# Kernel tuning notes

Hardware: AMD Instinct MI355X
Metric: run time of the kernel (lower is better)

## Reference

```python
import jax, jax.numpy as jnp
import numpy as np

N_NODES = 50000
N_EDGES = 800000
IN_DIM = 128
HID = 32
HEADS = 8
N_CLASSES = 10
N_GRAPHS = 64
NEG_SLOPE = 0.2


def _lin(key, fan_in, fan_out):
    return jax.random.normal(key, (fan_in, fan_out), jnp.float32) / np.sqrt(fan_in)


def setup_inputs() -> dict:
    key = jax.random.key(0)
    ks = jax.random.split(key, 24)
    x = jax.random.normal(ks[0], (N_NODES, IN_DIM), jnp.float32)
    edge_index = jax.random.randint(ks[1], (2, N_EDGES), 0, N_NODES, jnp.int64)
    batch = jnp.sort(jax.random.randint(ks[2], (N_NODES,), 0, N_GRAPHS, jnp.int64))
    HC = HEADS * HID
    return {
        "x": x,
        "edge_index": edge_index,
        "batch": batch,
        # GATConv(IN_DIM, HID, heads=8): shared lin, att_src/att_dst, bias on concat output
        "gat_W": _lin(ks[3], IN_DIM, HC),
        "gat_att_src": jax.random.normal(ks[4], (HEADS, HID), jnp.float32) / np.sqrt(HID),
        "gat_att_dst": jax.random.normal(ks[5], (HEADS, HID), jnp.float32) / np.sqrt(HID),
        "gat_b": jnp.zeros((HC,), jnp.float32),
        # GraphConv(HC, HID): lin_rel (bias) on aggregated neighbors + lin_root (no bias)
        "W2_rel": _lin(ks[6], HC, HID), "b2": jnp.zeros((HID,), jnp.float32), "W2_root": _lin(ks[7], HC, HID),
        # SAGEConv(HID, HID): lin_l (bias) on mean-aggregated neighbors + lin_r (no bias)
        "W3_l": _lin(ks[8], HID, HID), "b3": jnp.zeros((HID,), jnp.float32), "W3_r": _lin(ks[9], HID, HID),
        # GraphConv(HID, HID)
        "W4_rel": _lin(ks[10], HID, HID), "b4": jnp.zeros((HID,), jnp.float32), "W4_root": _lin(ks[11], HID, HID),
        "fc1_W": _lin(ks[12], HID, HID), "fc1_b": jnp.zeros((HID,), jnp.float32),
        "fc2_W": _lin(ks[13], HID, N_CLASSES), "fc2_b": jnp.zeros((N_CLASSES,), jnp.float32),
    }


def _segment_softmax(logits, seg_ids, num_segments):
    # numerically-stable softmax over edges grouped by destination node
    m = jax.ops.segment_max(logits, seg_ids, num_segments=num_segments)
    e = jnp.exp(logits - m[seg_ids])
    z = jax.ops.segment_sum(e, seg_ids, num_segments=num_segments)
    return e / (z[seg_ids] + 1e-16)


def _gnn_forward(x, edge_index, batch, gat_W, gat_att_src, gat_att_dst, gat_b,
                 W2_rel, b2, W2_root, W3_l, b3, W3_r, W4_rel, b4, W4_root,
                 fc1_W, fc1_b, fc2_W, fc2_b):
    N = x.shape[0]
    src0, dst0 = edge_index[0], edge_index[1]

    # ---- GATConv (PyG defaults: add_self_loops=True, concat heads, neg_slope=0.2) ----
    loops = jnp.arange(N)
    src = jnp.concatenate([src0, loops])
    dst = jnp.concatenate([dst0, loops])
    h = (x @ gat_W).reshape(N, HEADS, HID)                 # [N,H,C]
    a_src = jnp.sum(h * gat_att_src, axis=-1)              # [N,H]
    a_dst = jnp.sum(h * gat_att_dst, axis=-1)              # [N,H]
    logits = jax.nn.leaky_relu(a_src[src] + a_dst[dst], NEG_SLOPE)  # [E',H]
    alpha = _segment_softmax(logits, dst, N)               # [E',H]
    msg = h[src] * alpha[:, :, None]                       # [E',H,C]
    out = jax.ops.segment_sum(msg, dst, num_segments=N).reshape(N, HEADS * HID) + gat_b
    x1 = jax.nn.relu(out)

    # ---- GraphConv (aggr='add'): lin_rel(sum_j x_j) + lin_root(x) ----
    agg = jax.ops.segment_sum(x1[src0], dst0, num_segments=N)
    x2 = jax.nn.relu(agg @ W2_rel + b2 + x1 @ W2_root)

    # ---- SAGEConv (aggr='mean'): lin_l(mean_j x_j) + lin_r(x) ----
    deg = jax.ops.segment_sum(jnp.ones((src0.shape[0],), x2.dtype), dst0, num_segments=N)
    agg = jax.ops.segment_sum(x2[src0], dst0, num_segments=N) / jnp.clip(deg, 1.0)[:, None]
    x3 = jax.nn.relu(agg @ W3_l + b3 + x2 @ W3_r)

    # ---- GraphConv ----
    agg = jax.ops.segment_sum(x3[src0], dst0, num_segments=N)
    x4 = jax.nn.relu(agg @ W4_rel + b4 + x3 @ W4_root)

    # ---- global_mean_pool + MLP head ----
    gsum = jax.ops.segment_sum(x4, batch, num_segments=N_GRAPHS)
    gcnt = jax.ops.segment_sum(jnp.ones((N,), x4.dtype), batch, num_segments=N_GRAPHS)
    g = gsum / jnp.clip(gcnt, 1.0)[:, None]                # [G,HID]
    g = jax.nn.relu(g @ fc1_W + fc1_b)
    return g @ fc2_W + fc2_b                               # [G, N_CLASSES]


def reference(x, edge_index, batch, gat_W, gat_att_src, gat_att_dst, gat_b,
              W2_rel, b2, W2_root, W3_l, b3, W3_r, W4_rel, b4, W4_root,
              fc1_W, fc1_b, fc2_W, fc2_b):
    return _gnn_forward(x, edge_index, batch, gat_W, gat_att_src, gat_att_dst, gat_b,
                        W2_rel, b2, W2_root, W3_l, b3, W3_r, W4_rel, b4, W4_root,
                        fc1_W, fc1_b, fc2_W, fc2_b)
```

## Files before the change

### kernel.cpp

```cpp
#include <hip/hip_runtime.h>

#define IN_DIM 128
#define HID 32
#define HEADS 8
#define HC 256
#define N_GRAPHS 64
#define N_CLASSES 10

#define SCAN_ELEMS 8
#define SCAN_BLOCK 256
#define SCAN_CHUNK (SCAN_ELEMS * SCAN_BLOCK)

typedef __attribute__((ext_vector_type(8))) short bf16x8;
typedef __attribute__((ext_vector_type(4))) float f32x4;

__device__ __forceinline__ float leaky(float v) { return v > 0.f ? v : 0.2f * v; }

__device__ __forceinline__ unsigned fenc(float f) {
    unsigned u = __float_as_uint(f);
    return (u & 0x80000000u) ? ~u : (u | 0x80000000u);
}
__device__ __forceinline__ float fdec(unsigned u) {
    return __uint_as_float((u & 0x80000000u) ? (u & 0x7FFFFFFFu) : ~u);
}
__device__ __forceinline__ unsigned short bf16r(float f) {
    unsigned u = __float_as_uint(f);
    return (unsigned short)((u + 0x7FFFu + ((u >> 16) & 1u)) >> 16);
}
__device__ __forceinline__ float bdec(unsigned short u) {
    return __uint_as_float(((unsigned)u) << 16);
}

__global__ __launch_bounds__(256) void k_setup(
    int* __restrict__ deg, int N, unsigned* __restrict__ gm,
    float* __restrict__ gsum, float* __restrict__ gcnt, int* __restrict__ counter,
    const float* __restrict__ W, const float* __restrict__ Wrel, const float* __restrict__ Wroot,
    unsigned short* __restrict__ Wb, unsigned short* __restrict__ W2b)
{
    int i = blockIdx.x * 256 + threadIdx.x;
    if (i < N) deg[i] = 0;
    if (i < HEADS) gm[i] = 0u;
    if (i < N_GRAPHS * HID) gsum[i] = 0.f;
    if (i < N_GRAPHS) gcnt[i] = 0.f;
    if (i == 0) *counter = 0;

    if (blockIdx.x < 16) {
        int slot = blockIdx.x * 256 + threadIdx.x;
        int lane = slot & 63;
        int ctg  = (slot >> 6) & 15;
        int ks   = slot >> 10;
        int col  = ctg * 16 + (lane & 15);
        int kb   = ks * 32 + (lane >> 4) * 8;
        unsigned short t[8];
#pragma unroll
        for (int j = 0; j < 8; ++j) t[j] = bf16r(W[(size_t)(kb + j) * HC + col]);
        ushort4* dst = (ushort4*)(Wb + (size_t)slot * 8);
        dst[0] = make_ushort4(t[0], t[1], t[2], t[3]);
        dst[1] = make_ushort4(t[4], t[5], t[6], t[7]);
    } else if (blockIdx.x < 24) {
        int slot = (blockIdx.x - 16) * 256 + threadIdx.x;
        int lane = slot & 63;
        int ct   = (slot >> 6) & 3;
        int ks   = slot >> 8;
        int col  = ct * 16 + (lane & 15);
        int kb   = ks * 32 + (lane >> 4) * 8;
        const float* src = (col < HID) ? (Wrel + col) : (Wroot + (col - HID));
        unsigned short t[8];
#pragma unroll
        for (int j = 0; j < 8; ++j) t[j] = bf16r(src[(size_t)(kb + j) * HID]);
        ushort4* dst = (ushort4*)(W2b + (size_t)slot * 8);
        dst[0] = make_ushort4(t[0], t[1], t[2], t[3]);
        dst[1] = make_ushort4(t[4], t[5], t[6], t[7]);
    }
}

__global__ __launch_bounds__(256) void k_gemm_deg(
    const float* __restrict__ x, const unsigned short* __restrict__ Wb,
    const float* __restrict__ att_s, const float* __restrict__ att_d,
    unsigned short* __restrict__ h, float* __restrict__ a_src, float* __restrict__ a_dst, int N,
    const int* __restrict__ edst, int* __restrict__ deg, unsigned short* __restrict__ rank,
    int E, int gemmBlocks)
{
    __shared__ unsigned short sxt[16][136];
    __shared__ unsigned short sh[4][16][72];
    if (blockIdx.x >= gemmBlocks) {
        int i = (blockIdx.x - gemmBlocks) * 256 + threadIdx.x;
        if (i < E) rank[i] = (unsigned short)atomicAdd(&deg[edst[i]], 1);
        return;
    }
    int w = threadIdx.x >> 6;
    int lane = threadIdx.x & 63;
    int lrow = lane & 15, lgrp = lane >> 4;
    int nb = blockIdx.x * 16;

    {
        int row = threadIdx.x >> 4, col = (threadIdx.x & 15) * 8;
        int n = min(nb + row, N - 1);
        const float* xp = x + (size_t)n * IN_DIM + col;
        float4 a0 = *(const float4*)xp;
        float4 a1 = *(const float4*)(xp + 4);
        *(ushort4*)(&sxt[row][col])     = make_ushort4(bf16r(a0.x), bf16r(a0.y), bf16r(a0.z), bf16r(a0.w));
        *(ushort4*)(&sxt[row][col + 4]) = make_ushort4(bf16r(a1.x), bf16r(a1.y), bf16r(a1.z), bf16r(a1.w));
    }
    __syncthreads();

    f32x4 acc0 = {0.f, 0.f, 0.f, 0.f}, acc1 = acc0, acc2 = acc0, acc3 = acc0;

#pragma unroll
    for (int ks = 0; ks < 4; ++ks) {
        bf16x8 af = *(const bf16x8*)(&sxt[lrow][ks * 32 + lgrp * 8]);
        const bf16x8* bp = (const bf16x8*)(Wb + ((size_t)(ks * 16 + w * 4) * 64 + lane) * 8);
        acc0 = __builtin_amdgcn_mfma_f32_16x16x32_bf16(af, bp[0 * 64], acc0, 0, 0, 0);
        acc1 = __builtin_amdgcn_mfma_f32_16x16x32_bf16(af, bp[1 * 64], acc1, 0, 0, 0);
        acc2 = __builtin_amdgcn_mfma_f32_16x16x32_bf16(af, bp[2 * 64], acc2, 0, 0, 0);
        acc3 = __builtin_amdgcn_mfma_f32_16x16x32_bf16(af, bp[3 * 64], acc3, 0, 0, 0);
    }

    int cbase = w * 64;
#pragma unroll
    for (int r = 0; r < 4; ++r) {
        int lr = lgrp * 4 + r;
        sh[w][lr][lrow]      = bf16r(acc0[r]);
        sh[w][lr][16 + lrow] = bf16r(acc1[r]);
        sh[w][lr][32 + lrow] = bf16r(acc2[r]);
        sh[w][lr][48 + lrow] = bf16r(acc3[r]);
    }
#pragma unroll
    for (int round = 0; round < 2; ++round) {
        int row = (lane >> 3) + round * 8;
        int chunk = lane & 7;
        int n = nb + row;
        if (n < N) {
            uint4 t = *(const uint4*)(&sh[w][row][chunk * 8]);
            *(uint4*)(h + (size_t)n * HC + cbase + chunk * 8) = t;
        }
    }
    int h0 = cbase >> 5, h1 = h0 + 1;
    float as00 = att_s[h0 * HID + lrow], as01 = att_s[h0 * HID + 16 + lrow];
    float as10 = att_s[h1 * HID + lrow], as11 = att_s[h1 * HID + 16 + lrow];
    float ad00 = att_d[h0 * HID + lrow], ad01 = att_d[h0 * HID + 16 + lrow];
    float ad10 = att_d[h1 * HID + lrow], ad11 = att_d[h1 * HID + 16 + lrow];
#pragma unroll
    for (int r = 0; r < 4; ++r) {
        float ps0 = acc0[r] * as00 + acc1[r] * as01;
        float pd0 = acc0[r] * ad00 + acc1[r] * ad01;
        float ps1 = acc2[r] * as10 + acc3[r] * as11;
        float pd1 = acc2[r] * ad10 + acc3[r] * ad11;
#pragma unroll
        for (int d = 1; d < 16; d <<= 1) {
            ps0 += __shfl_xor(ps0, d); pd0 += __shfl_xor(pd0, d);
            ps1 += __shfl_xor(ps1, d); pd1 += __shfl_xor(pd1, d);
        }
        int n = nb + lgrp * 4 + r;
        if (lrow == 0 && n < N) {
            a_src[n * HEADS + h0] = ps0; a_dst[n * HEADS + h0] = pd0;
            a_src[n * HEADS + h1] = ps1; a_dst[n * HEADS + h1] = pd1;
        }
    }
}

__global__ __launch_bounds__(256) void k_amax_scan(
    const float* __restrict__ asrc, unsigned* __restrict__ gm, int N,
    const int* __restrict__ deg, int* __restrict__ bsum, int amaxBlocks)
{
    int tid = threadIdx.x;
    if (blockIdx.x < amaxBlocks) {
        __shared__ float sm[4][HEADS];
        float m[HEADS];
#pragma unroll
        for (int hh = 0; hh < HEADS; ++hh) m[hh] = -1e30f;
        int stride = amaxBlocks * 256;
        for (int n = blockIdx.x * 256 + tid; n < N; n += stride) {
            float4 p0 = *(const float4*)(asrc + (size_t)n * HEADS);
            float4 p1 = *(const float4*)(asrc + (size_t)n * HEADS + 4);
            m[0] = fmaxf(m[0], p0.x); m[1] = fmaxf(m[1], p0.y);
            m[2] = fmaxf(m[2], p0.z); m[3] = fmaxf(m[3], p0.w);
            m[4] = fmaxf(m[4], p1.x); m[5] = fmaxf(m[5], p1.y);
            m[6] = fmaxf(m[6], p1.z); m[7] = fmaxf(m[7], p1.w);
        }
#pragma unroll
        for (int hh = 0; hh < HEADS; ++hh)
            for (int d = 1; d < 64; d <<= 1) m[hh] = fmaxf(m[hh], __shfl_xor(m[hh], d));
        int lane = tid & 63, wv = tid >> 6;
        if (lane == 0)
#pragma unroll
            for (int hh = 0; hh < HEADS; ++hh) sm[wv][hh] = m[hh];
        __syncthreads();
        if (tid == 0) {
#pragma unroll
            for (int hh = 0; hh < HEADS; ++hh) {
                float mm = fmaxf(fmaxf(sm[0][hh], sm[1][hh]), fmaxf(sm[2][hh], sm[3][hh]));
                atomicMax(&gm[hh], fenc(mm));
            }
        }
    } else {
        int bid = blockIdx.x - amaxBlocks;
        int base = bid * SCAN_CHUNK + tid * SCAN_ELEMS;
        int s = 0;
#pragma unroll
        for (int i = 0; i < SCAN_ELEMS; ++i) { int idx = base + i; if (idx < N) s += deg[idx]; }
#pragma unroll
        for (int d = 1; d < 64; d <<= 1) s += __shfl_xor(s, d);
        __shared__ int ws[4];
        int lane = tid & 63, wv = tid >> 6;
        if (lane == 0) ws[wv] = s;
        __syncthreads();
        if (tid == 0) bsum[bid] = ws[0] + ws[1] + ws[2] + ws[3];
    }
}

__global__ __launch_bounds__(SCAN_BLOCK) void k_scan_write(
    const int* __restrict__ deg, const int* __restrict__ bsum,
    int* __restrict__ off, int N)
{
    __shared__ int sbpre;
    if (threadIdx.x < 64) {
        int lane = threadIdx.x;
        int bv = (lane < (int)blockIdx.x) ? bsum[lane] : 0;
        for (int d = 1; d < 64; d <<= 1) { int t = __shfl_up(bv, d); if (lane >= d) bv += t; }
        if (lane == 63) sbpre = bv;
    }
    int base = blockIdx.x * SCAN_CHUNK + threadIdx.x * SCAN_ELEMS;
    int dl[SCAN_ELEMS];
    int s = 0;
#pragma unroll
    for (int i = 0; i < SCAN_ELEMS; ++i) {
        int idx = base + i;
        dl[i] = (idx < N) ? deg[idx] : 0;
        s += dl[i];
    }
    int lane = threadIdx.x & 63, wv = threadIdx.x >> 6;
    int v = s;
#pragma unroll
    for (int d = 1; d < 64; d <<= 1) { int t = __shfl_up(v, d); if (lane >= d) v += t; }
    __shared__ int ws[4];
    if (lane == 63) ws[wv] = v;
    __syncthreads();
    int wadd = 0;
    for (int w = 0; w < wv; ++w) wadd += ws[w];
    int run = sbpre + wadd + (v - s);
#pragma unroll
    for (int i = 0; i < SCAN_ELEMS; ++i) {
        int idx = base + i;
        if (idx < N) {
            off[idx] = run;
            run += dl[i];
            if (idx == N - 1) off[N] = run;
        }
    }
}

__global__ void k_scatter(const int* __restrict__ src, const int* __restrict__ dst,
                          const unsigned short* __restrict__ rank, const int* __restrict__ off,
                          unsigned short* __restrict__ srcs, int E) {
    int i = blockIdx.x * blockDim.x + threadIdx.x;
    if (i < E) srcs[off[dst[i]] + (int)rank[i]] = (unsigned short)src[i];
}

__global__ __launch_bounds__(256) void k_gat_zr(
    const unsigned short* __restrict__ h, const float* __restrict__ asrc, const float* __restrict__ adst,
    const float* __restrict__ bias, const int* __restrict__ off, const unsigned short* __restrict__ srcs,
    const unsigned* __restrict__ gm, const unsigned short* __restrict__ W2b,
    unsigned short* __restrict__ z, unsigned short* __restrict__ rb, int N)
{
    __shared__ unsigned short sx1[16][264];
    int w = threadIdx.x >> 6;
    int lane = threadIdx.x & 63;
    int nb = blockIdx.x * 16;
    int head = lane >> 3;
    int c = lane * 4;
    float4 b4 = *(const float4*)(bias + c);
    float gmh = fdec(gm[head]);

    for (int t = 0; t < 4; ++t) {
        int v = min(nb + w * 4 + t, N - 1);
        float ad = adst[v * HEADS + head];
        float asv = asrc[v * HEADS + head];
        float m = leaky(gmh + ad);
        int beg = off[v], end = off[v + 1];

        ushort4 hv = *(const ushort4*)(h + (size_t)v * HC + c);
        float wg = __expf(leaky(asv + ad) - m);
        float zz = wg;
        float acc0 = wg * bdec(hv.x), acc1 = wg * bdec(hv.y), acc2 = wg * bdec(hv.z), acc3 = wg * bdec(hv.w);

        int e = beg;
        for (; e + 4 <= end; e += 4) {
            int s0 = srcs[e + 0], s1 = srcs[e + 1], s2 = srcs[e + 2], s3 = srcs[e + 3];
            float l0 = asrc[s0 * HEADS + head], l1 = asrc[s1 * HEADS + head];
            float l2 = asrc[s2 * HEADS + head], l3 = asrc[s3 * HEADS + head];
            ushort4 g0 = *(const ushort4*)(h + (size_t)s0 * HC + c);
            ushort4 g1 = *(const ushort4*)(h + (size_t)s1 * HC + c);
            ushort4 g2 = *(const ushort4*)(h + (size_t)s2 * HC + c);
            ushort4 g3 = *(const ushort4*)(h + (size_t)s3 * HC + c);
            float w0 = __expf(leaky(l0 + ad) - m);
            float w1 = __expf(leaky(l1 + ad) - m);
            float w2 = __expf(leaky(l2 + ad) - m);
            float w3 = __expf(leaky(l3 + ad) - m);
            zz += (w0 + w1) + (w2 + w3);
            acc0 += w0 * bdec(g0.x) + w1 * bdec(g1.x) + w2 * bdec(g2.x) + w3 * bdec(g3.x);
            acc1 += w0 * bdec(g0.y) + w1 * bdec(g1.y) + w2 * bdec(g2.y) + w3 * bdec(g3.y);
            acc2 += w0 * bdec(g0.z) + w1 * bdec(g1.z) + w2 * bdec(g2.z) + w3 * bdec(g3.z);
            acc3 += w0 * bdec(g0.w) + w1 * bdec(g1.w) + w2 * bdec(g2.w) + w3 * bdec(g3.w);
        }
        for (; e < end; ++e) {
            int s = srcs[e];
            float we = __expf(leaky(asrc[s * HEADS + head] + ad) - m);
            ushort4 hs = *(const ushort4*)(h + (size_t)s * HC + c);
            zz += we;
            acc0 += we * bdec(hs.x); acc1 += we * bdec(hs.y);
            acc2 += we * bdec(hs.z); acc3 += we * bdec(hs.w);
        }
        float inv_z = 1.f / (zz + 1e-16f);
        ushort4 o;
        o.x = bf16r(fmaxf(acc0 * inv_z + b4.x, 0.f));
        o.y = bf16r(fmaxf(acc1 * inv_z + b4.y, 0.f));
        o.z = bf16r(fmaxf(acc2 * inv_z + b4.z, 0.f));
        o.w = bf16r(fmaxf(acc3 * inv_z + b4.w, 0.f));
        *(ushort4*)(&sx1[w * 4 + t][c]) = o;
    }
    __syncthreads();

    int lrow = lane & 15, lgrp = lane >> 4;
    f32x4 acc = {0.f, 0.f, 0.f, 0.f};
#pragma unroll
    for (int ks = 0; ks < 8; ++ks) {
        bf16x8 af = *(const bf16x8*)(&sx1[lrow][ks * 32 + lgrp * 8]);
        const bf16x8* bp = (const bf16x8*)(W2b + ((size_t)(ks * 4 + w) * 64 + lane) * 8);
        acc = __builtin_amdgcn_mfma_f32_16x16x32_bf16(af, *bp, acc, 0, 0, 0);
    }
    int col = w * 16 + lrow;
#pragma unroll
    for (int rr = 0; rr < 4; ++rr) {
        int n = nb + lgrp * 4 + rr;
        if (n < N) {
            if (col < HID) z[(size_t)n * HID + col] = bf16r(acc[rr]);
            else           rb[(size_t)n * HID + (col - HID)] = bf16r(acc[rr]);
        }
    }
}

__global__ __launch_bounds__(256) void k_agg_lin(
    const unsigned short* __restrict__ z, const unsigned short* __restrict__ rb, const float* __restrict__ b,
    const int* __restrict__ off, const unsigned short* __restrict__ srcs,
    unsigned short* __restrict__ xout, int N)
{
    int nl = threadIdx.x >> 5, j = threadIdx.x & 31;
    int n = blockIdx.x * 8 + nl;
    if (n >= N) return;
    float acc = bdec(rb[n * HID + j]) + b[j];
    int beg = off[n], end = off[n + 1];
    int e = beg;
    for (; e + 8 <= end; e += 8) {
        int s0 = srcs[e], s1 = srcs[e + 1], s2 = srcs[e + 2], s3 = srcs[e + 3];
        int s4 = srcs[e + 4], s5 = srcs[e + 5], s6 = srcs[e + 6], s7 = srcs[e + 7];
        float v0 = bdec(z[s0 * HID + j]), v1 = bdec(z[s1 * HID + j]);
        float v2 = bdec(z[s2 * HID + j]), v3 = bdec(z[s3 * HID + j]);
        float v4 = bdec(z[s4 * HID + j]), v5 = bdec(z[s5 * HID + j]);
        float v6 = bdec(z[s6 * HID + j]), v7 = bdec(z[s7 * HID + j]);
        acc += ((v0 + v1) + (v2 + v3)) + ((v4 + v5) + (v6 + v7));
    }
    for (; e + 4 <= end; e += 4) {
        int s0 = srcs[e], s1 = srcs[e + 1], s2 = srcs[e + 2], s3 = srcs[e + 3];
        float v0 = bdec(z[s0 * HID + j]), v1 = bdec(z[s1 * HID + j]);
        float v2 = bdec(z[s2 * HID + j]), v3 = bdec(z[s3 * HID + j]);
        acc += (v0 + v1) + (v2 + v3);
    }
    for (; e < end; ++e)
        acc += bdec(z[srcs[e] * HID + j]);
    xout[n * HID + j] = bf16r(fmaxf(acc, 0.f));
}

template <bool MEAN>
__global__ __launch_bounds__(256) void k_conv32(
    const unsigned short* __restrict__ xin, const int* __restrict__ off, const unsigned short* __restrict__ srcs,
    const float* __restrict__ Wl, const float* __restrict__ Wr, const float* __restrict__ b,
    unsigned short* __restrict__ xout, int N)
{
    __shared__ float sagg[8][HID];
    __shared__ float sx[8][HID];
    int nl = threadIdx.x >> 5, j = threadIdx.x & 31;
    int n = blockIdx.x * 8 + nl;
    int nc = min(n, N - 1);
    int beg = off[nc], end = off[nc + 1];
    float acc = 0.f;
    int e = beg;
    for (; e + 8 <= end; e += 8) {
        int s0 = srcs[e], s1 = srcs[e + 1], s2 = srcs[e + 2], s3 = srcs[e + 3];
        int s4 = srcs[e + 4], s5 = srcs[e + 5], s6 = srcs[e + 6], s7 = srcs[e + 7];
        float v0 = bdec(xin[s0 * HID + j]), v1 = bdec(xin[s1 * HID + j]);
        float v2 = bdec(xin[s2 * HID + j]), v3 = bdec(xin[s3 * HID + j]);
        float v4 = bdec(xin[s4 * HID + j]), v5 = bdec(xin[s5 * HID + j]);
        float v6 = bdec(xin[s6 * HID + j]), v7 = bdec(xin[s7 * HID + j]);
        acc += ((v0 + v1) + (v2 + v3)) + ((v4 + v5) + (v6 + v7));
    }
    for (; e + 4 <= end; e += 4) {
        int s0 = srcs[e], s1 = srcs[e + 1], s2 = srcs[e + 2], s3 = srcs[e + 3];
        float v0 = bdec(xin[s0 * HID + j]), v1 = bdec(xin[s1 * HID + j]);
        float v2 = bdec(xin[s2 * HID + j]), v3 = bdec(xin[s3 * HID + j]);
        acc += (v0 + v1) + (v2 + v3);
    }
    for (; e < end; ++e)
        acc += bdec(xin[srcs[e] * HID + j]);
    if (MEAN) acc /= fmaxf((float)(end - beg), 1.f);
    sagg[nl][j] = acc;
    sx[nl][j] = bdec(xin[nc * HID + j]);
    __syncthreads();
    float o = b[j];
#pragma unroll
    for (int k = 0; k < HID; ++k)
        o += sagg[nl][k] * Wl[k * HID + j] + sx[nl][k] * Wr[k * HID + j];
    o = fmaxf(o, 0.f);
    if (n < N) xout[n * HID + j] = bf16r(o);
}

__global__ __launch_bounds__(256) void k_pool_head(
    const unsigned short* __restrict__ x4, const int* __restrict__ batch,
    float* __restrict__ gsum, float* __restrict__ gcnt, int N, int* __restrict__ counter,
    const float* __restrict__ fc1W, const float* __restrict__ fc1b,
    const float* __restrict__ fc2W, const float* __restrict__ fc2b,
    float* __restrict__ out)
{
    const int PER_BLOCK = 512;
    int base = blockIdx.x * PER_BLOCK;
    int endn = min(base + PER_BLOCK, N);
    int c = threadIdx.x & 31, no = threadIdx.x >> 5;
    {
        float acc = 0.f, cnt = 0.f;
        int curg = -1;
        for (int n = base + no; n < endn; n += 8) {
            int g = batch[n];
            if (g != curg) {
                if (curg >= 0) {
                    atomicAdd(&gsum[curg * HID + c], acc);
                    if (c == 0) atomicAdd(&gcnt[curg], cnt);
                }
                curg = g; acc = 0.f; cnt = 0.f;
            }
            acc += bdec(x4[n * HID + c]);
            cnt += 1.f;
        }
        if (curg >= 0) {
            atomicAdd(&gsum[curg * HID + c], acc);
            if (c == 0) atomicAdd(&gcnt[curg], cnt);
        }
    }
    __threadfence();
    __shared__ int lastFlag;
    if (threadIdx.x == 0) lastFlag = (atomicAdd(counter, 1) == (int)gridDim.x - 1);
    __syncthreads();
    if (!lastFlag) return;

    __shared__ float g[N_GRAPHS * HID];
    __shared__ float t[N_GRAPHS * HID];
    __shared__ float gc[N_GRAPHS];
    int tid = threadIdx.x;
    if (tid < N_GRAPHS) gc[tid] = atomicAdd(&gcnt[tid], 0.f);
    __syncthreads();
    for (int i = tid; i < N_GRAPHS * HID; i += 256)
        g[i] = atomicAdd(&gsum[i], 0.f) / fmaxf(gc[i >> 5], 1.f);
    __syncthreads();
    for (int i = tid; i < N_GRAPHS * HID; i += 256) {
        int gi = i >> 5, j = i & 31;
        float o = fc1b[j];
#pragma unroll
        for (int k = 0; k < HID; ++k) o += g[gi * HID + k] * fc1W[k * HID + j];
        t[i] = fmaxf(o, 0.f);
    }
    __syncthreads();
    for (int i = tid; i < N_GRAPHS * N_CLASSES; i += 256) {
        int gi = i / N_CLASSES, j = i % N_CLASSES;
        float o = fc2b[j];
#pragma unroll
        for (int k = 0; k < HID; ++k) o += t[gi * HID + k] * fc2W[k * N_CLASSES + j];
        out[i] = o;
    }
}

extern "C" void kernel_launch(void* const* d_in, const int* in_sizes, int n_in,
                              void* d_out, int out_size, void* d_ws, size_t ws_size,
                              hipStream_t stream)
{
    const float* x       = (const float*)d_in[0];
    const int*   eidx    = (const int*)d_in[1];
    const int*   batch   = (const int*)d_in[2];
    const float* gat_W   = (const float*)d_in[3];
    const float* att_s   = (const float*)d_in[4];
    const float* att_d   = (const float*)d_in[5];
    const float* gat_b   = (const float*)d_in[6];
    const float* W2_rel  = (const float*)d_in[7];
    const float* b2      = (const float*)d_in[8];
    const float* W2_root = (const float*)d_in[9];
    const float* W3_l    = (const float*)d_in[10];
    const float* b3      = (const float*)d_in[11];
    const float* W3_r    = (const float*)d_in[12];
    const float* W4_rel  = (const float*)d_in[13];
    const float* b4      = (const float*)d_in[14];
    const float* W4_root = (const float*)d_in[15];
    const float* fc1_W   = (const float*)d_in[16];
    const float* fc1_b   = (const float*)d_in[17];
    const float* fc2_W   = (const float*)d_in[18];
    const float* fc2_b   = (const float*)d_in[19];

    const int N = in_sizes[2];
    const int E = in_sizes[1] / 2;
    const int* esrc = eidx;
    const int* edst = eidx + E;

    char* wsb = (char*)d_ws;
    size_t ofs = 0;
    auto alloc = [&](size_t bytes) {
        char* p = wsb + ofs;
        ofs = (ofs + bytes + 255) & ~(size_t)255;
        return p;
    };
    unsigned short* h   = (unsigned short*)alloc((size_t)N * HC * 2);
    unsigned short* Wb  = (unsigned short*)alloc((size_t)IN_DIM * HC * 2);
    unsigned short* W2b = (unsigned short*)alloc((size_t)HC * 64 * 2);
    float* a_src = (float*)alloc((size_t)N * HEADS * 4);
    float* a_dst = (float*)alloc((size_t)N * HEADS * 4);
    int*   deg   = (int*)alloc((size_t)N * 4);
    int*   off   = (int*)alloc((size_t)(N + 1) * 4);
    unsigned short* rank = (unsigned short*)alloc((size_t)E * 2);
    unsigned short* srcs = (unsigned short*)alloc((size_t)E * 2);
    int*   bsum  = (int*)alloc((size_t)128 * 4);
    unsigned short* zb  = (unsigned short*)alloc((size_t)N * HID * 2);
    unsigned short* rb  = (unsigned short*)alloc((size_t)N * HID * 2);
    unsigned short* x2b = (unsigned short*)alloc((size_t)N * HID * 2);
    unsigned short* x3b = (unsigned short*)alloc((size_t)N * HID * 2);
    unsigned short* x4b = (unsigned short*)alloc((size_t)N * HID * 2);
    float* gsum  = (float*)alloc(N_GRAPHS * HID * 4);
    float* gcnt  = (float*)alloc(N_GRAPHS * 4);
    unsigned* gm = (unsigned*)alloc(HEADS * 4);
    int*  counter = (int*)alloc(4);
    (void)ws_size; (void)n_in; (void)out_size;

    const int nscan = (N + SCAN_CHUNK - 1) / SCAN_CHUNK;
    const int gemmBlocks = (N + 15) / 16;
    const int degBlocks  = (E + 255) / 256;
    const int amaxBlocks = 128;
    const int poolBlocks = (N + 511) / 512;

    k_setup<<<(N + 255) / 256, 256, 0, stream>>>(deg, N, gm, gsum, gcnt, counter,
                                                 gat_W, W2_rel, W2_root, Wb, W2b);
    k_gemm_deg<<<gemmBlocks + degBlocks, 256, 0, stream>>>(
        x, Wb, att_s, att_d, h, a_src, a_dst, N, edst, deg, rank, E, gemmBlocks);
    k_amax_scan<<<amaxBlocks + nscan, 256, 0, stream>>>(a_src, gm, N, deg, bsum, amaxBlocks);
    k_scan_write<<<nscan, SCAN_BLOCK, 0, stream>>>(deg, bsum, off, N);
    k_scatter<<<(E + 255) / 256, 256, 0, stream>>>(esrc, edst, rank, off, srcs, E);
    k_gat_zr<<<gemmBlocks, 256, 0, stream>>>(h, a_src, a_dst, gat_b, off, srcs, gm, W2b, zb, rb, N);
    k_agg_lin<<<(N + 7) / 8, 256, 0, stream>>>(zb, rb, b2, off, srcs, x2b, N);
    k_conv32<true><<<(N + 7) / 8, 256, 0, stream>>>(x2b, off, srcs, W3_l, W3_r, b3, x3b, N);
    k_conv32<false><<<(N + 7) / 8, 256, 0, stream>>>(x3b, off, srcs, W4_rel, W4_root, b4, x4b, N);
    k_pool_head<<<poolBlocks, 256, 0, stream>>>(x4b, batch, gsum, gcnt, N, counter,
                                                fc1_W, fc1_b, fc2_W, fc2_b, (float*)d_out);
}
```

Before: 270.3 us.

## Fuse tail GNN layers and pooling into one cooperative persistent kernel

Replaces the four tail kernels (GraphConv aggregation, SAGE conv, GraphConv, pooling plus MLP head) with a single cooperative kernel. It uses grid-wide syncs between stages and grid-stride loops over node tiles. This removes three kernel launches and the last-block counter, trading them for grid.sync barriers. Occupancy is now capped at a persistent grid, and the host makes occupancy and device-property queries on every launch.

```diff
diff --git a/kernel.cpp b/kernel.cpp
--- a/kernel.cpp
+++ b/kernel.cpp
@@ -1,4 +1,7 @@
 #include <hip/hip_runtime.h>
+#include <hip/hip_cooperative_groups.h>
+
+namespace cg = cooperative_groups;
 
 #define IN_DIM 128
 #define HID 32
@@ -33,7 +36,7 @@
 
 __global__ __launch_bounds__(256) void k_setup(
     int* __restrict__ deg, int N, unsigned* __restrict__ gm,
-    float* __restrict__ gsum, float* __restrict__ gcnt, int* __restrict__ counter,
+    float* __restrict__ gsum, float* __restrict__ gcnt,
     const float* __restrict__ W, const float* __restrict__ Wrel, const float* __restrict__ Wroot,
     unsigned short* __restrict__ Wb, unsigned short* __restrict__ W2b)
 {
@@ -42,7 +45,6 @@
     if (i < HEADS) gm[i] = 0u;
     if (i < N_GRAPHS * HID) gsum[i] = 0.f;
     if (i < N_GRAPHS) gcnt[i] = 0.f;
-    if (i == 0) *counter = 0;
 
     if (blockIdx.x < 16) {
         int slot = blockIdx.x * 256 + threadIdx.x;
@@ -340,47 +342,14 @@
     }
 }
 
-__global__ __launch_bounds__(256) void k_agg_lin(
-    const unsigned short* __restrict__ z, const unsigned short* __restrict__ rb, const float* __restrict__ b,
-    const int* __restrict__ off, const unsigned short* __restrict__ srcs,
-    unsigned short* __restrict__ xout, int N)
+__device__ __forceinline__ void conv32_body(
+    const unsigned short* __restrict__ xin, const int* __restrict__ off,
+    const unsigned short* __restrict__ srcs,
+    const float* __restrict__ Wl, const float* __restrict__ Wr, const float* __restrict__ b,
+    unsigned short* __restrict__ xout, int N, int tile, float* sagg, float* sx, bool mean)
 {
     int nl = threadIdx.x >> 5, j = threadIdx.x & 31;
-    int n = blockIdx.x * 8 + nl;
-    if (n >= N) return;
-    float acc = bdec(rb[n * HID + j]) + b[j];
-    int beg = off[n], end = off[n + 1];
-    int e = beg;
-    for (; e + 8 <= end; e += 8) {
-        int s0 = srcs[e], s1 = srcs[e + 1], s2 = srcs[e + 2], s3 = srcs[e + 3];
-        int s4 = srcs[e + 4], s5 = srcs[e + 5], s6 = srcs[e + 6], s7 = srcs[e + 7];
-        float v0 = bdec(z[s0 * HID + j]), v1 = bdec(z[s1 * HID + j]);
-        float v2 = bdec(z[s2 * HID + j]), v3 = bdec(z[s3 * HID + j]);
-        float v4 = bdec(z[s4 * HID + j]), v5 = bdec(z[s5 * HID + j]);
-        float v6 = bdec(z[s6 * HID + j]), v7 = bdec(z[s7 * HID + j]);
-        acc += ((v0 + v1) + (v2 + v3)) + ((v4 + v5) + (v6 + v7));
-    }
-    for (; e + 4 <= end; e += 4) {
-        int s0 = srcs[e], s1 = srcs[e + 1], s2 = srcs[e + 2], s3 = srcs[e + 3];
-        float v0 = bdec(z[s0 * HID + j]), v1 = bdec(z[s1 * HID + j]);
-        float v2 = bdec(z[s2 * HID + j]), v3 = bdec(z[s3 * HID + j]);
-        acc += (v0 + v1) + (v2 + v3);
-    }
-    for (; e < end; ++e)
-        acc += bdec(z[srcs[e] * HID + j]);
-    xout[n * HID + j] = bf16r(fmaxf(acc, 0.f));
-}
-
-template <bool MEAN>
-__global__ __launch_bounds__(256) void k_conv32(
-    const unsigned short* __restrict__ xin, const int* __restrict__ off, const unsigned short* __restrict__ srcs,
-    const float* __restrict__ Wl, const float* __restrict__ Wr, const float* __restrict__ b,
-    unsigned short* __restrict__ xout, int N)
-{
-    __shared__ float sagg[8][HID];
-    __shared__ float sx[8][HID];
-    int nl = threadIdx.x >> 5, j = threadIdx.x & 31;
-    int n = blockIdx.x * 8 + nl;
+    int n = tile * 8 + nl;
     int nc = min(n, N - 1);
     int beg = off[nc], end = off[nc + 1];
     float acc = 0.f;
@@ -402,78 +371,130 @@
     }
     for (; e < end; ++e)
         acc += bdec(xin[srcs[e] * HID + j]);
-    if (MEAN) acc /= fmaxf((float)(end - beg), 1.f);
-    sagg[nl][j] = acc;
-    sx[nl][j] = bdec(xin[nc * HID + j]);
+    if (mean) acc /= fmaxf((float)(end - beg), 1.f);
+    sagg[nl * HID + j] = acc;
+    sx[nl * HID + j] = bdec(xin[nc * HID + j]);
     __syncthreads();
     float o = b[j];
 #pragma unroll
     for (int k = 0; k < HID; ++k)
-        o += sagg[nl][k] * Wl[k * HID + j] + sx[nl][k] * Wr[k * HID + j];
+        o += sagg[nl * HID + k] * Wl[k * HID + j] + sx[nl * HID + k] * Wr[k * HID + j];
     o = fmaxf(o, 0.f);
     if (n < N) xout[n * HID + j] = bf16r(o);
-}
-
-__global__ __launch_bounds__(256) void k_pool_head(
-    const unsigned short* __restrict__ x4, const int* __restrict__ batch,
-    float* __restrict__ gsum, float* __restrict__ gcnt, int N, int* __restrict__ counter,
+    __syncthreads();
+}
+
+__global__ __launch_bounds__(256) void k_tail(
+    const unsigned short* __restrict__ zb, const unsigned short* __restrict__ rb,
+    const float* __restrict__ b2,
+    const int* __restrict__ off, const unsigned short* __restrict__ srcs,
+    unsigned short* __restrict__ x2b,
+    const float* __restrict__ W3l, const float* __restrict__ W3r, const float* __restrict__ b3,
+    unsigned short* __restrict__ x3b,
+    const float* __restrict__ W4l, const float* __restrict__ W4r, const float* __restrict__ b4,
+    unsigned short* __restrict__ x4b,
+    const int* __restrict__ batch, float* __restrict__ gsum, float* __restrict__ gcnt,
     const float* __restrict__ fc1W, const float* __restrict__ fc1b,
     const float* __restrict__ fc2W, const float* __restrict__ fc2b,
-    float* __restrict__ out)
-{
-    const int PER_BLOCK = 512;
-    int base = blockIdx.x * PER_BLOCK;
-    int endn = min(base + PER_BLOCK, N);
-    int c = threadIdx.x & 31, no = threadIdx.x >> 5;
+    float* __restrict__ out, int N)
+{
+    __shared__ float sbuf[4160];
+    cg::grid_group grid = cg::this_grid();
+    const int nT8 = (N + 7) / 8;
+
     {
-        float acc = 0.f, cnt = 0.f;
-        int curg = -1;
-        for (int n = base + no; n < endn; n += 8) {
-            int g = batch[n];
-            if (g != curg) {
-                if (curg >= 0) {
-                    atomicAdd(&gsum[curg * HID + c], acc);
-                    if (c == 0) atomicAdd(&gcnt[curg], cnt);
+        int nl = threadIdx.x >> 5, j = threadIdx.x & 31;
+        for (int t = blockIdx.x; t < nT8; t += gridDim.x) {
+            int n = t * 8 + nl;
+            if (n < N) {
+                float acc = bdec(rb[n * HID + j]) + b2[j];
+                int beg = off[n], end = off[n + 1];
+                int e = beg;
+                for (; e + 8 <= end; e += 8) {
+                    int s0 = srcs[e], s1 = srcs[e + 1], s2 = srcs[e + 2], s3 = srcs[e + 3];
+                    int s4 = srcs[e + 4], s5 = srcs[e + 5], s6 = srcs[e + 6], s7 = srcs[e + 7];
+                    float v0 = bdec(zb[s0 * HID + j]), v1 = bdec(zb[s1 * HID + j]);
+                    float v2 = bdec(zb[s2 * HID + j]), v3 = bdec(zb[s3 * HID + j]);
+                    float v4 = bdec(zb[s4 * HID + j]), v5 = bdec(zb[s5 * HID + j]);
+                    float v6 = bdec(zb[s6 * HID + j]), v7 = bdec(zb[s7 * HID + j]);
+                    acc += ((v0 + v1) + (v2 + v3)) + ((v4 + v5) + (v6 + v7));
                 }
-                curg = g; acc = 0.f; cnt = 0.f;
+                for (; e + 4 <= end; e += 4) {
+                    int s0 = srcs[e], s1 = srcs[e + 1], s2 = srcs[e + 2], s3 = srcs[e + 3];
+                    float v0 = bdec(zb[s0 * HID + j]), v1 = bdec(zb[s1 * HID + j]);
+                    float v2 = bdec(zb[s2 * HID + j]), v3 = bdec(zb[s3 * HID + j]);
+                    acc += (v0 + v1) + (v2 + v3);
+                }
+                for (; e < end; ++e)
+                    acc += bdec(zb[srcs[e] * HID + j]);
+                x2b[n * HID + j] = bf16r(fmaxf(acc, 0.f));
             }
-            acc += bdec(x4[n * HID + c]);
-            cnt += 1.f;
-        }
-        if (curg >= 0) {
-            atomicAdd(&gsum[curg * HID + c], acc);
-            if (c == 0) atomicAdd(&gcnt[curg], cnt);
-        }
-    }
-    __threadfence();
-    __shared__ int lastFlag;
-    if (threadIdx.x == 0) lastFlag = (atomicAdd(counter, 1) == (int)gridDim.x - 1);
-    __syncthreads();
-    if (!lastFlag) return;
-
-    __shared__ float g[N_GRAPHS * HID];
-    __shared__ float t[N_GRAPHS * HID];
-    __shared__ float gc[N_GRAPHS];
-    int tid = threadIdx.x;
-    if (tid < N_GRAPHS) gc[tid] = atomicAdd(&gcnt[tid], 0.f);
-    __syncthreads();
-    for (int i = tid; i < N_GRAPHS * HID; i += 256)
-        g[i] = atomicAdd(&gsum[i], 0.f) / fmaxf(gc[i >> 5], 1.f);
-    __syncthreads();
-    for (int i = tid; i < N_GRAPHS * HID; i += 256) {
-        int gi = i >> 5, j = i & 31;
-        float o = fc1b[j];
-#pragma unroll
-        for (int k = 0; k < HID; ++k) o += g[gi * HID + k] * fc1W[k * HID + j];
-        t[i] = fmaxf(o, 0.f);
-    }
-    __syncthreads();
-    for (int i = tid; i < N_GRAPHS * N_CLASSES; i += 256) {
-        int gi = i / N_CLASSES, j = i % N_CLASSES;
-        float o = fc2b[j];
-#pragma unroll
-        for (int k = 0; k < HID; ++k) o += t[gi * HID + k] * fc2W[k * N_CLASSES + j];
-        out[i] = o;
+        }
+    }
+    grid.sync();
+
+    for (int t = blockIdx.x; t < nT8; t += gridDim.x)
+        conv32_body(x2b, off, srcs, W3l, W3r, b3, x3b, N, t, sbuf, sbuf + 256, true);
+    grid.sync();
+
+    for (int t = blockIdx.x; t < nT8; t += gridDim.x)
+        conv32_body(x3b, off, srcs, W4l, W4r, b4, x4b, N, t, sbuf, sbuf + 256, false);
+    grid.sync();
+
+    {
+        const int PER_BLOCK = 512;
+        int nChunks = (N + PER_BLOCK - 1) / PER_BLOCK;
+        int c = threadIdx.x & 31, no = threadIdx.x >> 5;
+        for (int ch = blockIdx.x; ch < nChunks; ch += gridDim.x) {
+            int base = ch * PER_BLOCK;
+            int endn = min(base + PER_BLOCK, N);
+            float acc = 0.f, cnt = 0.f;
+            int curg = -1;
+            for (int n = base + no; n < endn; n += 8) {
+                int g = batch[n];
+                if (g != curg) {
+                    if (curg >= 0) {
+                        atomicAdd(&gsum[curg * HID + c], acc);
+                        if (c == 0) atomicAdd(&gcnt[curg], cnt);
+                    }
+                    curg = g; acc = 0.f; cnt = 0.f;
+                }
+                acc += bdec(x4b[n * HID + c]);
+                cnt += 1.f;
+            }
+            if (curg >= 0) {
+                atomicAdd(&gsum[curg * HID + c], acc);
+                if (c == 0) atomicAdd(&gcnt[curg], cnt);
+            }
+        }
+    }
+    grid.sync();
+
+    if (blockIdx.x == 0) {
+        float* g  = sbuf;
+        float* t  = sbuf + 2048;
+        float* gc = sbuf + 4096;
+        int tid = threadIdx.x;
+        if (tid < N_GRAPHS) gc[tid] = atomicAdd(&gcnt[tid], 0.f);
+        __syncthreads();
+        for (int i = tid; i < N_GRAPHS * HID; i += 256)
+            g[i] = atomicAdd(&gsum[i], 0.f) / fmaxf(gc[i >> 5], 1.f);
+        __syncthreads();
+        for (int i = tid; i < N_GRAPHS * HID; i += 256) {
+            int gi = i >> 5, j = i & 31;
+            float o = fc1b[j];
+#pragma unroll
+            for (int k = 0; k < HID; ++k) o += g[gi * HID + k] * fc1W[k * HID + j];
+            t[i] = fmaxf(o, 0.f);
+        }
+        __syncthreads();
+        for (int i = tid; i < N_GRAPHS * N_CLASSES; i += 256) {
+            int gi = i / N_CLASSES, j = i % N_CLASSES;
+            float o = fc2b[j];
+#pragma unroll
+            for (int k = 0; k < HID; ++k) o += t[gi * HID + k] * fc2W[k * N_CLASSES + j];
+            out[i] = o;
+        }
     }
 }
 
@@ -532,16 +553,24 @@
     float* gsum  = (float*)alloc(N_GRAPHS * HID * 4);
     float* gcnt  = (float*)alloc(N_GRAPHS * 4);
     unsigned* gm = (unsigned*)alloc(HEADS * 4);
-    int*  counter = (int*)alloc(4);
     (void)ws_size; (void)n_in; (void)out_size;
 
     const int nscan = (N + SCAN_CHUNK - 1) / SCAN_CHUNK;
     const int gemmBlocks = (N + 15) / 16;
     const int degBlocks  = (E + 255) / 256;
     const int amaxBlocks = 128;
-    const int poolBlocks = (N + 511) / 512;
-
-    k_setup<<<(N + 255) / 256, 256, 0, stream>>>(deg, N, gm, gsum, gcnt, counter,
+
+    int maxBpc = 0;
+    hipOccupancyMaxActiveBlocksPerMultiprocessor(&maxBpc, k_tail, 256, 0);
+    if (maxBpc < 1) maxBpc = 1;
+    hipDeviceProp_t prop;
+    int dev = 0;
+    hipGetDevice(&dev);
+    hipGetDeviceProperties(&prop, dev);
+    int coopGrid = maxBpc * prop.multiProcessorCount;
+    if (coopGrid < 64) coopGrid = 64;
+
+    k_setup<<<(N + 255) / 256, 256, 0, stream>>>(deg, N, gm, gsum, gcnt,
                                                  gat_W, W2_rel, W2_root, Wb, W2b);
     k_gemm_deg<<<gemmBlocks + degBlocks, 256, 0, stream>>>(
         x, Wb, att_s, att_d, h, a_src, a_dst, N, edst, deg, rank, E, gemmBlocks);
@@ -549,9 +578,19 @@
     k_scan_write<<<nscan, SCAN_BLOCK, 0, stream>>>(deg, bsum, off, N);
     k_scatter<<<(E + 255) / 256, 256, 0, stream>>>(esrc, edst, rank, off, srcs, E);
     k_gat_zr<<<gemmBlocks, 256, 0, stream>>>(h, a_src, a_dst, gat_b, off, srcs, gm, W2b, zb, rb, N);
-    k_agg_lin<<<(N + 7) / 8, 256, 0, stream>>>(zb, rb, b2, off, srcs, x2b, N);
-    k_conv32<true><<<(N + 7) / 8, 256, 0, stream>>>(x2b, off, srcs, W3_l, W3_r, b3, x3b, N);
-    k_conv32<false><<<(N + 7) / 8, 256, 0, stream>>>(x3b, off, srcs, W4_rel, W4_root, b4, x4b, N);
-    k_pool_head<<<poolBlocks, 256, 0, stream>>>(x4b, batch, gsum, gcnt, N, counter,
-                                                fc1_W, fc1_b, fc2_W, fc2_b, (float*)d_out);
-}
+
+    int Nv = N;
+    void* args[] = {
+        (void*)&zb, (void*)&rb, (void*)&b2, (void*)&off, (void*)&srcs,
+        (void*)&x2b, (void*)&W3_l, (void*)&W3_r, (void*)&b3, (void*)&x3b,
+        (void*)&W4_rel, (void*)&b4, (void*)&W4_root, (void*)&x4b,
+        (void*)&batch, (void*)&gsum, (void*)&gcnt,
+        (void*)&fc1_W, (void*)&fc1_b, (void*)&fc2_W, (void*)&fc2_b,
+        (void*)&d_out, (void*)&Nv
+    };
+    args[10] = (void*)&W4_rel;
+    args[11] = (void*)&W4_root;
+    args[12] = (void*)&b4;
+    args[13] = (void*)&x4b;
+    hipLaunchCooperativeKernel((void*)k_tail, dim3(coopGrid), dim3(256), args, 0, stream);
+}
```

Result: slower. 566.4 us (+109.5%).
